# Performance work log

Measured on AMD Instinct MI355X. Metric: run time of the kernel, lower is better.

## Reference

```python
import jax, jax.numpy as jnp
import numpy as np

NH = 8        # num_heads
KS = 64       # key_size
C_IN = 256
C_OUT = 3 * NH * KS   # 1536
GROUPS = 3 * NH       # 24
EPS = 1e-5
H = W = 64


def setup_inputs() -> dict:
    key = jax.random.key(0)
    k1, k2 = jax.random.split(key)
    x = jax.random.normal(k1, (1, C_IN, H, W), dtype=jnp.float32)
    conv_w = jax.random.normal(k2, (C_OUT, C_IN, 1, 1), dtype=jnp.float32) * 0.05
    gn_w = jnp.ones((C_OUT,), dtype=jnp.float32)
    gn_b = jnp.zeros((C_OUT,), dtype=jnp.float32)
    return {"x": x, "conv_w": conv_w, "gn_w": gn_w, "gn_b": gn_b}


def reference(x, conv_w, gn_w, gn_b):
    B, _, h, w = x.shape
    # 1x1 conv (normalize=True -> no bias): per-pixel GEMM over channels
    attn = jnp.einsum('bchw,oc->bohw', x, conv_w[:, :, 0, 0])  # [B, 1536, H, W]
    # GroupNorm: 24 groups of KS channels, normalized over (KS, H, W)
    g = attn.reshape(B, GROUPS, -1)
    mean = g.mean(axis=-1, keepdims=True)
    var = g.var(axis=-1, keepdims=True)
    g = (g - mean) * jax.lax.rsqrt(var + EPS)
    attn = g.reshape(B, C_OUT, h, w) * gn_w[None, :, None, None] + gn_b[None, :, None, None]
    # split into key, query, value (in that order, per chunk(3, dim=2))
    attn = attn.reshape(B, NH, 3 * KS, h * w)
    key_, query, value = jnp.split(attn, 3, axis=2)   # each [B, NH, KS, HW]
    # saliency = q^T @ k / sqrt(KS) -> [B, NH, HW, HW]
    saliency = jnp.einsum('bnkq,bnkl->bnql', query, key_) / jnp.sqrt(jnp.float32(KS))
    mask = jax.nn.softmax(saliency, axis=-1)
    # out = v @ mask^T -> [B, NH, KS, HW]
    out = jnp.einsum('bnkl,bnql->bnkq', value, mask)
    return out.reshape(B, NH * KS, h, w)
```

## Files before the change

kernel.cpp:

```cpp
#include <hip/hip_runtime.h>

typedef __bf16 bf16;
typedef __bf16 bf16x8 __attribute__((ext_vector_type(8)));
typedef __bf16 bf16x4 __attribute__((ext_vector_type(4)));
typedef float f32x4 __attribute__((ext_vector_type(4)));
typedef float f32x16 __attribute__((ext_vector_type(16)));


#define QF 0.18033688011112042f
#define EXPF(x) __builtin_amdgcn_exp2f(x)

union U4 { bf16x4 v; unsigned u[2]; };
union U8 { bf16x8 v; unsigned u[4]; };

__global__ void k_misc(const float* __restrict__ x, const float* __restrict__ w,
                       bf16* __restrict__ xT, bf16* __restrict__ wb, float* __restrict__ cs) {
    int b = blockIdx.x;
    if (b < 512) {
        int t = b * 256 + threadIdx.x;
        int p  = t & 4095;
        int c0 = (t >> 12) * 8;
        bf16x8 o;
#pragma unroll
        for (int j = 0; j < 8; j++) o[j] = (bf16)x[(c0 + j) * 4096 + p];
        *(bf16x8*)(xT + p * 256 + c0) = o;
    } else if (b < 896) {
        int idx = ((b - 512) * 256 + threadIdx.x) * 4;
        float4 f = *(const float4*)(w + idx);
        bf16x4 o;
        o[0] = (bf16)f.x; o[1] = (bf16)f.y; o[2] = (bf16)f.z; o[3] = (bf16)f.w;
        *(bf16x4*)(wb + idx) = o;
    } else {
#pragma unroll
        for (int i = 0; i < 12; i++) cs[i * 256 + threadIdx.x] = 0.f;
    }
}

__global__ __launch_bounds__(256) void k_conv(const bf16* __restrict__ Wb,
                                              const bf16* __restrict__ xT,
                                              bf16* __restrict__ qkvT,
                                              float* __restrict__ cs) {
    __shared__ __attribute__((aligned(16))) bf16 tile[64 * 72];
    int wid = threadIdx.x >> 6, lane = threadIdx.x & 63;
    int quad = lane >> 4, l15 = lane & 15;
    int g  = blockIdx.x % 24;
    int pb = (blockIdx.x / 24) * 64;
    int h = g / 3, sec = g % 3;
    int ob = g * 64;
    int orow = ob + wid * 16 + l15;

    f32x4 acc[4];
#pragma unroll
    for (int c = 0; c < 4; c++) acc[c] = (f32x4){0.f, 0.f, 0.f, 0.f};

#pragma unroll
    for (int ks = 0; ks < 8; ks++) {
        bf16x8 a = *(const bf16x8*)(Wb + orow * 256 + ks * 32 + quad * 8);
#pragma unroll
        for (int c = 0; c < 4; c++) {
            bf16x8 b = *(const bf16x8*)(xT + (pb + c * 16 + l15) * 256 + ks * 32 + quad * 8);
            acc[c] = __builtin_amdgcn_mfma_f32_16x16x32_bf16(a, b, acc[c], 0, 0, 0);
        }
    }

    int ch0 = wid * 16 + quad * 4;
#pragma unroll
    for (int r = 0; r < 4; r++) {
        float sp  = acc[0][r] + acc[1][r] + acc[2][r] + acc[3][r];
        float ssp = acc[0][r] * acc[0][r] + acc[1][r] * acc[1][r]
                  + acc[2][r] * acc[2][r] + acc[3][r] * acc[3][r];
#pragma unroll
        for (int m = 1; m < 16; m <<= 1) {
            sp  += __shfl_xor(sp,  m, 64);
            ssp += __shfl_xor(ssp, m, 64);
        }
        if (l15 == 0) {
            atomicAdd(cs + (ob + ch0 + r) * 2,     sp);
            atomicAdd(cs + (ob + ch0 + r) * 2 + 1, ssp);
        }
    }

    if (sec == 2) {
#pragma unroll
        for (int c = 0; c < 4; c++)
#pragma unroll
            for (int r = 0; r < 4; r++)
                tile[(ch0 + r) * 72 + c * 16 + l15] = (bf16)acc[c][r];
    } else {
#pragma unroll
        for (int c = 0; c < 4; c++) {
            bf16x4 o;
#pragma unroll
            for (int r = 0; r < 4; r++) o[r] = (bf16)acc[c][r];
            *(bf16x4*)(&tile[(c * 16 + l15) * 72 + ch0]) = o;
        }
    }
    __syncthreads();
    bf16* base = qkvT + h * 786432;
    int t = threadIdx.x;
    if (sec == 2) {
        bf16* V = base + 524288;
#pragma unroll
        for (int it = 0; it < 2; it++) {
            int e = it * 256 + t; int ch = e >> 3; int pxo = (e & 7) * 8;
            *(bf16x8*)(V + ch * 4096 + pb + pxo) = *(const bf16x8*)(&tile[ch * 72 + pxo]);
        }
    } else {
        bf16* dst = base + (sec == 0 ? 262144 : 0);
#pragma unroll
        for (int it = 0; it < 2; it++) {
            int e = it * 256 + t; int px = e >> 3; int cho = (e & 7) * 8;
            *(bf16x8*)(dst + (pb + px) * 64 + cho) = *(const bf16x8*)(&tile[px * 72 + cho]);
        }
    }
}

__global__ __launch_bounds__(256) void k_normqk(bf16* __restrict__ qkv,
                                                const float2* __restrict__ cs,
                                                const float* __restrict__ gnw,
                                                const float* __restrict__ gnb) {
    int h    = blockIdx.x >> 8;
    int base = (blockIdx.x & 255) * 2048;
    int isQ  = base < 262144;
    int g    = h * 3 + (isQ ? 1 : 0);

    int c = threadIdx.x & 63;
    float2 v = cs[g * 64 + c];
    float s = v.x, ss = v.y;
#pragma unroll
    for (int m = 1; m < 64; m <<= 1) { s += __shfl_xor(s, m, 64); ss += __shfl_xor(ss, m, 64); }
    const float N = 262144.0f;
    float mean = s / N;
    float inv  = rsqrtf(ss / N - mean * mean + 1e-5f);
    float f = isQ ? QF : 1.0f;

    int e = base + threadIdx.x * 8;
    int gc = h * 192 + (isQ ? 64 : 0) + (e & 63);
    bf16* p = qkv + h * 786432 + e;
    bf16x8 vv = *(bf16x8*)p;
    bf16x8 o;
#pragma unroll
    for (int j = 0; j < 8; j++) {
        float gw = gnw[gc + j];
        float a = inv * gw * f;
        float b = (gnb[gc + j] - mean * inv * gw) * f;
        o[j] = (bf16)(a * (float)vv[j] + b);
    }
    *(bf16x8*)p = o;
}

#define PF_BLOCK(S, PFA, PFB)                                                   \
    {                                                                           \
        float p0 = EXPF(S[0]),  p1 = EXPF(S[1]),  p2 = EXPF(S[2]),  p3 = EXPF(S[3]);   \
        float p4 = EXPF(S[4]),  p5 = EXPF(S[5]),  p6 = EXPF(S[6]),  p7 = EXPF(S[7]);   \
        float p8 = EXPF(S[8]),  p9 = EXPF(S[9]),  p10 = EXPF(S[10]), p11 = EXPF(S[11]); \
        float p12 = EXPF(S[12]), p13 = EXPF(S[13]), p14 = EXPF(S[14]), p15 = EXPF(S[15]); \
        lacc += (((p0 + p1) + (p2 + p3)) + ((p4 + p5) + (p6 + p7)))             \
              + (((p8 + p9) + (p10 + p11)) + ((p12 + p13) + (p14 + p15)));      \
        U4 lo, hi;                                                              \
        lo.v[0] = (bf16)p0;  lo.v[1] = (bf16)p1;  lo.v[2] = (bf16)p2;  lo.v[3] = (bf16)p3;  \
        hi.v[0] = (bf16)p4;  hi.v[1] = (bf16)p5;  hi.v[2] = (bf16)p6;  hi.v[3] = (bf16)p7;  \
        unsigned sa = half ? lo.u[0] : hi.u[0];                                 \
        unsigned sb = half ? lo.u[1] : hi.u[1];                                 \
        unsigned ra = (unsigned)__shfl_xor((int)sa, 32, 64);                    \
        unsigned rb = (unsigned)__shfl_xor((int)sb, 32, 64);                    \
        U8 fA;                                                                  \
        fA.u[0] = half ? ra : lo.u[0];  fA.u[1] = half ? rb : lo.u[1];          \
        fA.u[2] = half ? hi.u[0] : ra;  fA.u[3] = half ? hi.u[1] : rb;          \
        PFA = fA.v;                                                             \
        U4 lo2, hi2;                                                            \
        lo2.v[0] = (bf16)p8;  lo2.v[1] = (bf16)p9;  lo2.v[2] = (bf16)p10; lo2.v[3] = (bf16)p11; \
        hi2.v[0] = (bf16)p12; hi2.v[1] = (bf16)p13; hi2.v[2] = (bf16)p14; hi2.v[3] = (bf16)p15; \
        unsigned sc = half ? lo2.u[0] : hi2.u[0];                               \
        unsigned sd = half ? lo2.u[1] : hi2.u[1];                               \
        unsigned rc = (unsigned)__shfl_xor((int)sc, 32, 64);                    \
        unsigned rd = (unsigned)__shfl_xor((int)sd, 32, 64);                    \
        U8 fB;                                                                  \
        fB.u[0] = half ? rc : lo2.u[0];  fB.u[1] = half ? rd : lo2.u[1];        \
        fB.u[2] = half ? hi2.u[0] : rc;  fB.u[3] = half ? hi2.u[1] : rd;        \
        PFB = fB.v;                                                             \
    }

__global__ __launch_bounds__(256, 3) void k_attn(const bf16* __restrict__ qkvT,
                                                 bf16* __restrict__ Opart,
                                                 float* __restrict__ Lsum) {
    int bid   = blockIdx.x;
    int h     = bid & 7;
    int qb    = (bid >> 3) & 31;
    int split = bid >> 8;
    int wid = threadIdx.x >> 6, lane = threadIdx.x & 63;
    int l31 = lane & 31, half = lane >> 5;
    const bf16* QT = qkvT + h * 786432;
    const bf16* KT = QT + 262144;
    const bf16* V  = QT + 524288;
    int qw = qb * 128 + wid * 32;

    __shared__ __attribute__((aligned(16))) bf16 Ks[64 * 72];
    __shared__ __attribute__((aligned(16))) bf16 Vs[64 * 72];

    int r0   = threadIdx.x >> 3;
    int koff = (threadIdx.x & 7) * 8;

    bf16x8 bq[4];
#pragma unroll
    for (int ks = 0; ks < 4; ks++)
        bq[ks] = *(const bf16x8*)(QT + (qw + l31) * 64 + ks * 16 + half * 8);

    f32x16 oacc0 = (f32x16)(0.0f), oacc1 = (f32x16)(0.0f);
    float ls = 0.f;

    int t0 = (split * 64) / 3, t1 = ((split + 1) * 64) / 3;

    bf16x8 kf0, kf1, vf0, vf1;
    {
        int lb0 = t0 * 64;
        kf0 = *(const bf16x8*)(KT + (lb0 + r0) * 64 + koff);
        kf1 = *(const bf16x8*)(KT + (lb0 + r0 + 32) * 64 + koff);
        vf0 = *(const bf16x8*)(V + r0 * 4096 + lb0 + koff);
        vf1 = *(const bf16x8*)(V + (r0 + 32) * 4096 + lb0 + koff);
    }

    for (int lt = t0; lt < t1; lt++) {
        __syncthreads();
        *(bf16x8*)(Ks + r0 * 72 + koff)        = kf0;
        *(bf16x8*)(Ks + (r0 + 32) * 72 + koff) = kf1;
        *(bf16x8*)(Vs + r0 * 72 + koff)        = vf0;
        *(bf16x8*)(Vs + (r0 + 32) * 72 + koff) = vf1;
        __syncthreads();

        if (lt + 1 < t1) {
            int nb = (lt + 1) * 64;
            kf0 = *(const bf16x8*)(KT + (nb + r0) * 64 + koff);
            kf1 = *(const bf16x8*)(KT + (nb + r0 + 32) * 64 + koff);
            vf0 = *(const bf16x8*)(V + r0 * 4096 + nb + koff);
            vf1 = *(const bf16x8*)(V + (r0 + 32) * 4096 + nb + koff);
        }

        f32x16 s0 = (f32x16)(0.0f), s1 = (f32x16)(0.0f);
#pragma unroll
        for (int ks = 0; ks < 4; ks++) {
            s0 = __builtin_amdgcn_mfma_f32_32x32x16_bf16(
                *(const bf16x8*)(Ks + l31 * 72 + ks * 16 + half * 8), bq[ks], s0, 0, 0, 0);
            s1 = __builtin_amdgcn_mfma_f32_32x32x16_bf16(
                *(const bf16x8*)(Ks + (32 + l31) * 72 + ks * 16 + half * 8), bq[ks], s1, 0, 0, 0);
        }

        float lacc = ls;
        bf16x8 pf0, pf1, pf2, pf3;
        PF_BLOCK(s0, pf0, pf1);
        PF_BLOCK(s1, pf2, pf3);
        ls = lacc;

        oacc0 = __builtin_amdgcn_mfma_f32_32x32x16_bf16(
            *(const bf16x8*)(Vs + l31 * 72 +  0 + half * 8), pf0, oacc0, 0, 0, 0);
        oacc1 = __builtin_amdgcn_mfma_f32_32x32x16_bf16(
            *(const bf16x8*)(Vs + (32 + l31) * 72 +  0 + half * 8), pf0, oacc1, 0, 0, 0);
        oacc0 = __builtin_amdgcn_mfma_f32_32x32x16_bf16(
            *(const bf16x8*)(Vs + l31 * 72 + 16 + half * 8), pf1, oacc0, 0, 0, 0);
        oacc1 = __builtin_amdgcn_mfma_f32_32x32x16_bf16(
            *(const bf16x8*)(Vs + (32 + l31) * 72 + 16 + half * 8), pf1, oacc1, 0, 0, 0);
        oacc0 = __builtin_amdgcn_mfma_f32_32x32x16_bf16(
            *(const bf16x8*)(Vs + l31 * 72 + 32 + half * 8), pf2, oacc0, 0, 0, 0);
        oacc1 = __builtin_amdgcn_mfma_f32_32x32x16_bf16(
            *(const bf16x8*)(Vs + (32 + l31) * 72 + 32 + half * 8), pf2, oacc1, 0, 0, 0);
        oacc0 = __builtin_amdgcn_mfma_f32_32x32x16_bf16(
            *(const bf16x8*)(Vs + l31 * 72 + 48 + half * 8), pf3, oacc0, 0, 0, 0);
        oacc1 = __builtin_amdgcn_mfma_f32_32x32x16_bf16(
            *(const bf16x8*)(Vs + (32 + l31) * 72 + 48 + half * 8), pf3, oacc1, 0, 0, 0);
    }

    ls += __shfl_xor(ls, 32, 64);
    if (half == 0)
        Lsum[split * 32768 + h * 4096 + qw + l31] = ls;

    bf16* Ob = Opart + split * 2097152;
#pragma unroll
    for (int r = 0; r < 16; r++) {
        int kd = (r & 3) + 8 * (r >> 2) + 4 * half;
        Ob[(h * 64 + kd) * 4096 + qw + l31]        = (bf16)oacc0[r];
        Ob[(h * 64 + 32 + kd) * 4096 + qw + l31]   = (bf16)oacc1[r];
    }
}

__global__ void k_final(const bf16* __restrict__ Opart, const float* __restrict__ Lsum,
                        const float2* __restrict__ cs, const float* __restrict__ gnw,
                        const float* __restrict__ gnb, float* __restrict__ out) {
    int gid = blockIdx.x * 256 + threadIdx.x;
    int row = gid >> 9;
    int c8  = (gid & 511) << 3;
    int h   = row >> 6;

    int g = h * 3 + 2;
    int c = threadIdx.x & 63;
    float2 v = cs[g * 64 + c];
    float s = v.x, ss = v.y;
#pragma unroll
    for (int m = 1; m < 64; m <<= 1) { s += __shfl_xor(s, m, 64); ss += __shfl_xor(ss, m, 64); }
    const float N = 262144.0f;
    float mean = s / N;
    float inv  = rsqrtf(ss / N - mean * mean + 1e-5f);
    int gi = h * 192 + 128 + (row & 63);
    float gw = gnw[gi];
    float va = inv * gw;
    float vb = gnb[gi] - mean * inv * gw;

    float o[8] = {0, 0, 0, 0, 0, 0, 0, 0};
    float l[8] = {0, 0, 0, 0, 0, 0, 0, 0};
#pragma unroll
    for (int sp = 0; sp < 3; sp++) {
        bf16x8 vv = *(const bf16x8*)(Opart + sp * 2097152 + row * 4096 + c8);
        const float* L = Lsum + sp * 32768 + h * 4096 + c8;
        float4 l0 = *(const float4*)L;
        float4 l1 = *(const float4*)(L + 4);
#pragma unroll
        for (int j = 0; j < 8; j++) o[j] += (float)vv[j];
        l[0] += l0.x; l[1] += l0.y; l[2] += l0.z; l[3] += l0.w;
        l[4] += l1.x; l[5] += l1.y; l[6] += l1.z; l[7] += l1.w;
    }
    float4 r0, r1;
    r0.x = va * o[0] / l[0] + vb; r0.y = va * o[1] / l[1] + vb;
    r0.z = va * o[2] / l[2] + vb; r0.w = va * o[3] / l[3] + vb;
    r1.x = va * o[4] / l[4] + vb; r1.y = va * o[5] / l[5] + vb;
    r1.z = va * o[6] / l[6] + vb; r1.w = va * o[7] / l[7] + vb;
    *(float4*)(out + row * 4096 + c8)     = r0;
    *(float4*)(out + row * 4096 + c8 + 4) = r1;
}

extern "C" void kernel_launch(void* const* d_in, const int* in_sizes, int n_in,
                              void* d_out, int out_size, void* d_ws, size_t ws_size,
                              hipStream_t stream) {
    const float* x      = (const float*)d_in[0];
    const float* conv_w = (const float*)d_in[1];
    const float* gn_w   = (const float*)d_in[2];
    const float* gn_b   = (const float*)d_in[3];
    float* out = (float*)d_out;
    char* ws = (char*)d_ws;

    bf16*   qkvT  = (bf16*) (ws);
    bf16*   Opart = (bf16*) (ws + 12582912);
    bf16*   Wb    = (bf16*) (ws + 12582912);
    bf16*   xT    = (bf16*) (ws + 13369344);
    float*  Lsum  = (float*)(ws + 25165824);
    float*  cs    = (float*)(ws + 25559040);

    hipLaunchKernelGGL(k_misc,   dim3(897),  dim3(256), 0, stream, x, conv_w, xT, Wb, cs);
    hipLaunchKernelGGL(k_conv,   dim3(1536), dim3(256), 0, stream, Wb, xT, qkvT, cs);
    hipLaunchKernelGGL(k_normqk, dim3(2048), dim3(256), 0, stream, qkvT, (const float2*)cs, gn_w, gn_b);
    hipLaunchKernelGGL(k_attn,   dim3(768),  dim3(256), 0, stream, qkvT, Opart, Lsum);
    hipLaunchKernelGGL(k_final,  dim3(1024), dim3(256), 0, stream, Opart, Lsum, (const float2*)cs, gn_w, gn_b, out);
}
```

Measured before the change: 155.5 us.

## Stage conv GEMM operands through LDS with register prefetch

The 1x1-conv GEMM kernel now loads 64-channel slices of x and W cooperatively into shared memory, with coalesced 16-element rows per thread, instead of each wave reading its fragments straight from global memory. The next slice is prefetched into registers while MFMAs run on the current one. This removes the duplicate global reads of the xT tile across the four waves and improves coalescing. In exchange it adds LDS traffic, a second LDS buffer, and two barriers per channel slice. A barrier is added before the tile reuse in the epilogue.

Measured after the change: 141.5 us. 1.1x faster.

```diff
diff --git a/kernel.cpp b/kernel.cpp
--- a/kernel.cpp
+++ b/kernel.cpp
@@ -40,26 +40,51 @@
                                               const bf16* __restrict__ xT,
                                               bf16* __restrict__ qkvT,
                                               float* __restrict__ cs) {
-    __shared__ __attribute__((aligned(16))) bf16 tile[64 * 72];
+    __shared__ __attribute__((aligned(16))) bf16 xs[64 * 72];
+    __shared__ __attribute__((aligned(16))) bf16 ws2[64 * 72];
     int wid = threadIdx.x >> 6, lane = threadIdx.x & 63;
     int quad = lane >> 4, l15 = lane & 15;
     int g  = blockIdx.x % 24;
     int pb = (blockIdx.x / 24) * 64;
     int h = g / 3, sec = g % 3;
     int ob = g * 64;
-    int orow = ob + wid * 16 + l15;
+
+    int srow = threadIdx.x >> 2;
+    int scol = (threadIdx.x & 3) * 16;
 
     f32x4 acc[4];
 #pragma unroll
     for (int c = 0; c < 4; c++) acc[c] = (f32x4){0.f, 0.f, 0.f, 0.f};
 
-#pragma unroll
-    for (int ks = 0; ks < 8; ks++) {
-        bf16x8 a = *(const bf16x8*)(Wb + orow * 256 + ks * 32 + quad * 8);
-#pragma unroll
-        for (int c = 0; c < 4; c++) {
-            bf16x8 b = *(const bf16x8*)(xT + (pb + c * 16 + l15) * 256 + ks * 32 + quad * 8);
-            acc[c] = __builtin_amdgcn_mfma_f32_16x16x32_bf16(a, b, acc[c], 0, 0, 0);
+    bf16x8 fx0 = *(const bf16x8*)(xT + (pb + srow) * 256 + scol);
+    bf16x8 fx1 = *(const bf16x8*)(xT + (pb + srow) * 256 + scol + 8);
+    bf16x8 fw0 = *(const bf16x8*)(Wb + (ob + srow) * 256 + scol);
+    bf16x8 fw1 = *(const bf16x8*)(Wb + (ob + srow) * 256 + scol + 8);
+
+    for (int c4 = 0; c4 < 4; c4++) {
+        __syncthreads();
+        *(bf16x8*)(xs  + srow * 72 + scol)     = fx0;
+        *(bf16x8*)(xs  + srow * 72 + scol + 8) = fx1;
+        *(bf16x8*)(ws2 + srow * 72 + scol)     = fw0;
+        *(bf16x8*)(ws2 + srow * 72 + scol + 8) = fw1;
+        __syncthreads();
+
+        if (c4 < 3) {
+            int co = (c4 + 1) * 64;
+            fx0 = *(const bf16x8*)(xT + (pb + srow) * 256 + co + scol);
+            fx1 = *(const bf16x8*)(xT + (pb + srow) * 256 + co + scol + 8);
+            fw0 = *(const bf16x8*)(Wb + (ob + srow) * 256 + co + scol);
+            fw1 = *(const bf16x8*)(Wb + (ob + srow) * 256 + co + scol + 8);
+        }
+
+#pragma unroll
+        for (int k2 = 0; k2 < 2; k2++) {
+            bf16x8 a = *(const bf16x8*)(ws2 + (wid * 16 + l15) * 72 + k2 * 32 + quad * 8);
+#pragma unroll
+            for (int c = 0; c < 4; c++) {
+                bf16x8 b = *(const bf16x8*)(xs + (c * 16 + l15) * 72 + k2 * 32 + quad * 8);
+                acc[c] = __builtin_amdgcn_mfma_f32_16x16x32_bf16(a, b, acc[c], 0, 0, 0);
+            }
         }
     }
 
@@ -80,6 +105,8 @@
         }
     }
 
+    __syncthreads();
+    bf16* tile = xs;
     if (sec == 2) {
 #pragma unroll
         for (int c = 0; c < 4; c++)
```
